# Performance work log

Hardware: AMD Instinct MI355X
Metric: run time of the kernel (lower is better)

## Reference

```python
import jax, jax.numpy as jnp
import numpy as np
import math

N_HEADS = 32
N_KV_HEADS = 8
MAX_SEQ_LEN = 2048


def _rope_cos_sin(seq_len, head_dim, dtype):
    # precompute_freqs_cis: theta=10000, positions 0..seq_len-1 (note: NOT offset by start_pos, faithful to source)
    inv_freq = 1.0 / (10000.0 ** (jnp.arange(0, head_dim, 2, dtype=jnp.float32) / head_dim))
    t = jnp.arange(seq_len, dtype=jnp.float32)
    angles = jnp.outer(t, inv_freq)  # [S, hd/2]
    return jnp.cos(angles).astype(dtype), jnp.sin(angles).astype(dtype)


def _apply_rope(x, cos, sin):
    # x: [B, S, H, hd]; rotate consecutive pairs (llama complex convention)
    B, S, H, hd = x.shape
    xr = x.reshape(B, S, H, hd // 2, 2)
    x1, x2 = xr[..., 0], xr[..., 1]
    c = cos[None, :, None, :]
    s = sin[None, :, None, :]
    o1 = x1 * c - x2 * s
    o2 = x1 * s + x2 * c
    return jnp.stack([o1, o2], axis=-1).reshape(B, S, H, hd)


def setup_inputs() -> dict:
    key = jax.random.key(0)
    ks = jax.random.split(key, 5)
    dim = 4096
    B, S = 1, 2048
    sd = 1.0 / math.sqrt(dim)
    return {
        "x": jax.random.normal(ks[0], (B, S, dim), dtype=jnp.float32),
        "wq": jax.random.normal(ks[1], (4096, 4096), dtype=jnp.float32) * sd,
        "wk": jax.random.normal(ks[2], (1024, 4096), dtype=jnp.float32) * sd,
        "wv": jax.random.normal(ks[3], (1024, 4096), dtype=jnp.float32) * sd,
        "wo": jax.random.normal(ks[4], (4096, 4096), dtype=jnp.float32) * sd,
        "start_pos": 0,
    }


def reference(x, wq, wk, wv, wo, start_pos):
    B, S, D = x.shape
    Hq, Hkv = N_HEADS, N_KV_HEADS
    hd = D // Hq
    n_rep = Hq // Hkv

    xq = (x @ wq.T).reshape(B, S, Hq, hd)
    xk = (x @ wk.T).reshape(B, S, Hkv, hd)
    xv = (x @ wv.T).reshape(B, S, Hkv, hd)

    cos, sin = _rope_cos_sin(S, hd, x.dtype)
    xq = _apply_rope(xq, cos, sin)
    xk = _apply_rope(xk, cos, sin)

    # KV cache append + read back [:, :start_pos+S] (start_pos is a static Python int)
    cache_k = jnp.zeros((B, MAX_SEQ_LEN, Hkv, hd), dtype=x.dtype)
    cache_v = jnp.zeros((B, MAX_SEQ_LEN, Hkv, hd), dtype=x.dtype)
    cache_k = jax.lax.dynamic_update_slice(cache_k, xk, (0, start_pos, 0, 0))
    cache_v = jax.lax.dynamic_update_slice(cache_v, xv, (0, start_pos, 0, 0))
    kv_len = start_pos + S
    keys = cache_k[:, :kv_len]    # [B, K, Hkv, hd]
    values = cache_v[:, :kv_len]

    # GQA repeat_kv: [B, K, Hkv, hd] -> [B, K, Hq, hd]
    keys = jnp.broadcast_to(keys[:, :, :, None, :], (B, kv_len, Hkv, n_rep, hd)).reshape(B, kv_len, Hq, hd)
    values = jnp.broadcast_to(values[:, :, :, None, :], (B, kv_len, Hkv, n_rep, hd)).reshape(B, kv_len, Hq, hd)

    scale = 1.0 / math.sqrt(hd)
    scores = jnp.einsum('bqhd,bkhd->bhqk', xq, keys) * scale  # [B, Hq, S, K]
    # NOTE: source applies NO causal mask — faithful reproduction
    attn = jax.nn.softmax(scores, axis=-1)
    out = jnp.einsum('bhqk,bkhd->bqhd', attn, values).reshape(B, S, Hq * hd)
    return out @ wo.T
```

## Files before the change

### kernel.cpp

```cpp
#include <hip/hip_runtime.h>
#include <hip/hip_bf16.h>

typedef _Float16 f16_t;
typedef unsigned int uint;
typedef __attribute__((ext_vector_type(8))) _Float16 f16x8;
typedef __attribute__((ext_vector_type(4))) _Float16 f16x4;
typedef __attribute__((ext_vector_type(4))) float f32x4;
typedef __attribute__((ext_vector_type(16))) float f32x16;

#define ROPE_C (13.287712379549449f / 64.0f)

__global__ __launch_bounds__(256) void repack_x16(const float* __restrict__ src,
                                                  uint16_t* __restrict__ dh)
{
    const int p  = blockIdx.y;
    const int kb = blockIdx.x;
    const int tid = threadIdx.x;
    const int rr = tid >> 3;
    const int k4 = tid & 7;
    const int slot = k4 >> 1;
    const int so   = (k4 & 1) * 4;
    uint16_t* bh = dh + ((size_t)p * 128 + kb) * 4096;
    #pragma unroll
    for (int it = 0; it < 4; ++it) {
        const int r = it * 32 + rr;
        const float4 v = *reinterpret_cast<const float4*>(
            &src[((size_t)p * 128 + r) * 4096 + kb * 32 + k4 * 4]);
        float f[4] = {v.x, v.y, v.z, v.w};
        f16x4 h;
        #pragma unroll
        for (int e = 0; e < 4; ++e) h[e] = (f16_t)f[e];
        const int pos = r * 32 + ((slot ^ ((r >> 1) & 3)) << 3) + so;
        *reinterpret_cast<f16x4*>(&bh[pos]) = h;
    }
}

__global__ __launch_bounds__(256) void repack_w96_16(const float* __restrict__ wq,
                                                     const float* __restrict__ wk,
                                                     const float* __restrict__ wv,
                                                     uint16_t* __restrict__ dst)
{
    const int kb  = blockIdx.x;
    const int pan = blockIdx.y;
    const int tid = threadIdx.x;
    const int k4 = tid & 7;
    const int slot = k4 >> 1;
    const int so   = (k4 & 1) * 4;
    uint16_t* bh = dst + ((size_t)pan * 128 + kb) * 3072;
    #pragma unroll
    for (int it = 0; it < 3; ++it) {
        const int r = it * 32 + (tid >> 3);
        const int n = pan * 96 + r;
        const float* srow = (n < 4096) ? (wq + (size_t)n * 4096)
                          : (n < 5120) ? (wk + (size_t)(n - 4096) * 4096)
                                       : (wv + (size_t)(n - 5120) * 4096);
        const float4 v = *reinterpret_cast<const float4*>(srow + kb * 32 + k4 * 4);
        float f[4] = {v.x, v.y, v.z, v.w};
        f16x4 h;
        #pragma unroll
        for (int e = 0; e < 4; ++e) h[e] = (f16_t)f[e];
        const int pos = r * 32 + ((slot ^ ((r >> 1) & 3)) << 3) + so;
        *reinterpret_cast<f16x4*>(&bh[pos]) = h;
    }
}

__global__ __launch_bounds__(256) void repack_h16(const float* __restrict__ src,
                                                  uint16_t* __restrict__ dh)
{
    const int p  = blockIdx.y;
    const int kb = blockIdx.x;
    const int tid = threadIdx.x;
    const int rr = tid >> 3;
    const int k4 = tid & 7;
    const int slot = k4 >> 1;
    const int so   = (k4 & 1) * 4;
    uint16_t* bh = dh + ((size_t)p * 128 + kb) * 4096;
    #pragma unroll
    for (int it = 0; it < 4; ++it) {
        const int r = it * 32 + rr;
        const float4 v = *reinterpret_cast<const float4*>(
            &src[((size_t)p * 128 + r) * 4096 + kb * 32 + k4 * 4]);
        float f[4] = {v.x, v.y, v.z, v.w};
        f16x4 h;
        #pragma unroll
        for (int e = 0; e < 4; ++e) h[e] = (f16_t)f[e];
        const int pos = r * 32 + ((slot ^ ((r >> 1) & 3)) << 3) + so;
        *reinterpret_cast<f16x4*>(&bh[pos]) = h;
    }
}

__global__ __launch_bounds__(512) void gemm_qkv9(const uint16_t* __restrict__ xh,
                                                 const uint16_t* __restrict__ wqkv,
                                                 uint16_t* __restrict__ xq16,
                                                 uint16_t* __restrict__ xk16,
                                                 uint16_t* __restrict__ xv16)
{
    __shared__ char lds[2][40960];

    const int bid = blockIdx.x;
    const int swz = (bid & 7) * 64 + (bid >> 3);
    const int by = swz >> 5;
    const int bx = swz & 31;
    const int tid = threadIdx.x;
    const int w = tid >> 6, lane = tid & 63;
    const int wm = w >> 2, wn = w & 3;
    const int fr = lane & 15, s4 = lane >> 4;

    const uint16_t* sp[5];
    int dof[5];
    int stridec[5];
    #pragma unroll
    for (int i = 0; i < 5; ++i) {
        const int c = w + 8 * i;
        if (c < 16) {
            const int kk = c >> 3, inner = c & 7;
            sp[i] = xh + (size_t)by * 524288 + kk * 4096 + inner * 512 + lane * 8;
            dof[i] = c * 1024;
            stridec[i] = 8192;
        } else {
            const int cb = c - 16;
            const int pan = cb / 12, rem = cb % 12;
            const int kk = rem / 6, inner = rem % 6;
            sp[i] = wqkv + (size_t)(bx * 2 + pan) * 393216 + kk * 3072 + inner * 512 + lane * 8;
            dof[i] = 16384 + cb * 1024;
            stridec[i] = 6144;
        }
    }

    f32x4 acc[4][3] = {};

    #pragma unroll
    for (int i = 0; i < 5; ++i)
        __builtin_amdgcn_global_load_lds(
            (const __attribute__((address_space(1))) void*)(sp[i]),
            (__attribute__((address_space(3))) void*)(&lds[0][0] + dof[i]), 16, 0, 0);
    asm volatile("s_waitcnt vmcnt(0)" ::: "memory");
    __builtin_amdgcn_s_barrier();
    __builtin_amdgcn_sched_barrier(0);

    for (int t = 0; t < 64; ++t) {
        const char* b = &lds[t & 1][0];
        if (t + 1 < 64) {
            char* nb = &lds[(t + 1) & 1][0];
            #pragma unroll
            for (int i = 0; i < 5; ++i)
                __builtin_amdgcn_global_load_lds(
                    (const __attribute__((address_space(1))) void*)(sp[i] + (size_t)(t + 1) * stridec[i]),
                    (__attribute__((address_space(3))) void*)(nb + dof[i]), 16, 0, 0);
        }
        #pragma unroll
        for (int kk = 0; kk < 2; ++kk) {
            f16x8 fb[3];
            #pragma unroll
            for (int j = 0; j < 3; ++j) {
                const int cbp = wn * 48 + j * 16 + fr;
                const int pan = (cbp >= 96) ? 1 : 0;
                const int rb = cbp - pan * 96;
                fb[j] = *reinterpret_cast<const f16x8*>(
                    b + 16384 + pan * 12288 + kk * 6144 + rb * 64 + ((s4 ^ ((rb >> 1) & 3)) << 4));
            }
            #pragma unroll
            for (int ri = 0; ri < 4; ++ri) {
                const int rloc = wm * 64 + ri * 16 + fr;
                f16x8 fh = *reinterpret_cast<const f16x8*>(
                    b + kk * 8192 + rloc * 64 + ((s4 ^ ((rloc >> 1) & 3)) << 4));
                __builtin_amdgcn_s_setprio(1);
                #pragma unroll
                for (int j = 0; j < 3; ++j)
                    acc[ri][j] = __builtin_amdgcn_mfma_f32_16x16x32_f16(fh, fb[j], acc[ri][j], 0, 0, 0);
                __builtin_amdgcn_s_setprio(0);
            }
        }
        asm volatile("s_waitcnt vmcnt(0)" ::: "memory");
        __builtin_amdgcn_s_barrier();
        __builtin_amdgcn_sched_barrier(0);
    }

    const int r0 = by * 128 + wm * 64 + s4 * 4;
    const int c0 = bx * 192 + wn * 48 + fr;
    #pragma unroll
    for (int ri = 0; ri < 4; ++ri)
        #pragma unroll
        for (int j = 0; j < 3; ++j) {
            const int col = c0 + j * 16;
            #pragma unroll
            for (int rr = 0; rr < 4; ++rr) {
                const int row = r0 + ri * 16 + rr;
                const f16_t v = (f16_t)acc[ri][j][rr];
                uint16_t bits;
                __builtin_memcpy(&bits, &v, 2);
                if (col < 4096)      xq16[(size_t)row * 4096 + col] = bits;
                else if (col < 5120) xk16[(size_t)row * 1024 + (col - 4096)] = bits;
                else                 xv16[(size_t)row * 1024 + (col - 5120)] = bits;
            }
        }
}

__global__ __launch_bounds__(512) void gemm_out8(const uint16_t* __restrict__ aoh,
                                                 const uint16_t* __restrict__ woh,
                                                 float* __restrict__ out)
{
    __shared__ char lds[2][49152];

    const int bid = blockIdx.x;
    const int swz = (bid & 7) * 32 + (bid >> 3);
    const int by = swz >> 5;
    const int bx = swz & 31;
    const int tid = threadIdx.x;
    const int w = tid >> 6, lane = tid & 63;
    const int wm = w >> 2, wn = w & 3;
    const int fr = lane & 15, s4 = lane >> 4;

    const uint16_t* sp[6];
    int dof[6];
    #pragma unroll
    for (int i = 0; i < 6; ++i) {
        const int c = w + 8 * i;
        if (c < 32) {
            const int pan = c >> 4, sub = c & 15;
            sp[i] = aoh + (size_t)(2 * by + pan) * 524288 + sub * 512 + lane * 8;
            dof[i] = c * 1024;
        } else {
            sp[i] = woh + (size_t)bx * 524288 + (c - 32) * 512 + lane * 8;
            dof[i] = 32768 + (c - 32) * 1024;
        }
    }

    f32x4 acc[8][2] = {};

    #pragma unroll
    for (int i = 0; i < 6; ++i)
        __builtin_amdgcn_global_load_lds(
            (const __attribute__((address_space(1))) void*)(sp[i]),
            (__attribute__((address_space(3))) void*)(&lds[0][0] + dof[i]), 16, 0, 0);
    asm volatile("s_waitcnt vmcnt(0)" ::: "memory");
    __builtin_amdgcn_s_barrier();
    __builtin_amdgcn_sched_barrier(0);

    for (int t = 0; t < 64; ++t) {
        const char* b = &lds[t & 1][0];
        if (t + 1 < 64) {
            char* nb = &lds[(t + 1) & 1][0];
            #pragma unroll
            for (int i = 0; i < 6; ++i)
                __builtin_amdgcn_global_load_lds(
                    (const __attribute__((address_space(1))) void*)(sp[i] + (size_t)(t + 1) * 8192),
                    (__attribute__((address_space(3))) void*)(nb + dof[i]), 16, 0, 0);
        }
        #pragma unroll
        for (int kk = 0; kk < 2; ++kk) {
            f16x8 fb[2];
            #pragma unroll
            for (int j = 0; j < 2; ++j) {
                const int cbp = wn * 32 + j * 16 + fr;
                fb[j] = *reinterpret_cast<const f16x8*>(
                    b + 32768 + kk * 8192 + cbp * 64 + ((s4 ^ ((cbp >> 1) & 3)) << 4));
            }
            #pragma unroll
            for (int p = 0; p < 4; ++p) {
                f16x8 fh[2];
                #pragma unroll
                for (int f = 0; f < 2; ++f) {
                    const int rloc = p * 32 + f * 16 + fr;
                    fh[f] = *reinterpret_cast<const f16x8*>(
                        b + wm * 16384 + kk * 8192 + rloc * 64 + ((s4 ^ ((rloc >> 1) & 3)) << 4));
                }
                __builtin_amdgcn_s_setprio(1);
                #pragma unroll
                for (int f = 0; f < 2; ++f)
                    #pragma unroll
                    for (int j = 0; j < 2; ++j)
                        acc[p * 2 + f][j] = __builtin_amdgcn_mfma_f32_16x16x32_f16(fh[f], fb[j], acc[p * 2 + f][j], 0, 0, 0);
                __builtin_amdgcn_s_setprio(0);
            }
        }
        asm volatile("s_waitcnt vmcnt(0)" ::: "memory");
        __builtin_amdgcn_s_barrier();
        __builtin_amdgcn_sched_barrier(0);
    }

    const int r0 = by * 256 + wm * 128 + s4 * 4;
    const int c0 = bx * 128 + wn * 32 + fr;
    #pragma unroll
    for (int ri = 0; ri < 8; ++ri)
        #pragma unroll
        for (int j = 0; j < 2; ++j)
            #pragma unroll
            for (int rr = 0; rr < 4; ++rr)
                out[(size_t)(r0 + ri * 16 + rr) * 4096 + c0 + j * 16] = acc[ri][j][rr];
}

__global__ __launch_bounds__(256) void conv_kv(const uint16_t* __restrict__ xk16,
                                               const uint16_t* __restrict__ xv16,
                                               uint16_t* __restrict__ kvg)
{
    __shared__ float V[32][129];
    const int t = blockIdx.x;
    const int h = blockIdx.y;
    const int tid = threadIdx.x;
    uint16_t* tile = kvg + ((size_t)(h * 64 + t)) * 8192;

    #pragma unroll
    for (int i = 0; i < 4; ++i) {
        const int v = i * 256 + tid;
        const int row = v >> 5, c4 = (v & 31) * 4;
        f16x4 hv = *reinterpret_cast<const f16x4*>(&xv16[(size_t)(t * 32 + row) * 1024 + h * 128 + c4]);
        #pragma unroll
        for (int e = 0; e < 4; ++e) V[row][c4 + e] = (float)hv[e];
    }

    {
        const int r = tid >> 3;
        const int d0 = (tid & 7) * 16;
        const int pos_ = t * 32 + r;
        float f[16];
        const uint16_t* kr = &xk16[(size_t)pos_ * 1024 + h * 128 + d0];
        f16x8 k0 = *reinterpret_cast<const f16x8*>(kr);
        f16x8 k1 = *reinterpret_cast<const f16x8*>(kr + 8);
        #pragma unroll
        for (int e = 0; e < 8; ++e) { f[e] = (float)k0[e]; f[8 + e] = (float)k1[e]; }
        #pragma unroll
        for (int i = 0; i < 8; ++i) {
            const int j = (d0 >> 1) + i;
            const float invf = exp2f(-(float)j * ROPE_C);
            const float ang = (float)pos_ * invf;
            float sn, cs;
            __sincosf(ang, &sn, &cs);
            const float x1 = f[2 * i], x2 = f[2 * i + 1];
            f[2 * i]     = x1 * cs - x2 * sn;
            f[2 * i + 1] = x1 * sn + x2 * cs;
        }
        #pragma unroll
        for (int cc = 0; cc < 2; ++cc) {
            f16x8 hv;
            #pragma unroll
            for (int e = 0; e < 8; ++e) hv[e] = (f16_t)f[cc * 8 + e];
            const int c = (d0 >> 3) + cc;
            const int pos = r * 128 + ((c ^ (r & 15)) << 3);
            *reinterpret_cast<f16x8*>(&tile[pos]) = hv;
        }
    }
    __syncthreads();
    {
        const int d = tid >> 1;
        const int k0 = (tid & 1) * 16;
        float g[16];
        #pragma unroll
        for (int j = 0; j < 16; ++j) g[j] = V[k0 + j][d];
        #pragma unroll
        for (int cc = 0; cc < 2; ++cc) {
            f16x8 hv;
            #pragma unroll
            for (int e = 0; e < 8; ++e) hv[e] = (f16_t)g[cc * 8 + e];
            const int c = (k0 >> 3) + cc;
            const int pos = 4096 + d * 32 + ((c ^ (d & 3)) << 3);
            *reinterpret_cast<f16x8*>(&tile[pos]) = hv;
        }
    }
}

__device__ __forceinline__ uint cvtpkh(float lo, float hi) {
    uint r;
    asm("v_cvt_pkrtz_f16_f32 %0, %1, %2" : "=v"(r) : "v"(lo), "v"(hi));
    return r;
}
__device__ __forceinline__ void permswap(uint& a, uint& b) {
    asm("v_permlane32_swap_b32 %0, %1" : "+v"(a), "+v"(b));
}
__device__ __forceinline__ f16x8 pack4h(uint w0, uint w1, uint w2, uint w3) {
    union { uint u[4]; f16x8 v; } t;
    t.u[0] = w0; t.u[1] = w1; t.u[2] = w2; t.u[3] = w3;
    return t.v;
}

__global__ __launch_bounds__(512, 2) void attn_mfma(const uint16_t* __restrict__ xq16,
                                                    const uint16_t* __restrict__ kvg,
                                                    uint16_t* __restrict__ aoh)
{
    __shared__ char lds[2][16384];

    const int b = blockIdx.x;
    const int kvh = b & 7;
    const int r = b >> 3;
    const int h = kvh * 4 + (r & 3);
    const int q0 = (r >> 2) * 256;
    const int tid = threadIdx.x;
    const int w = tid >> 6;
    const int lane = tid & 63;
    const int ln31 = lane & 31;
    const int hi = lane >> 5;

    const int q = q0 + w * 32 + ln31;
    const uint16_t* qrow = xq16 + (size_t)q * 4096 + h * 128;
    f16x8 Qh[8];
    #pragma unroll
    for (int ks = 0; ks < 8; ++ks) {
        const int dbase = ks * 16 + hi * 8;
        f16x8 raw = *reinterpret_cast<const f16x8*>(qrow + dbase);
        float f[8];
        #pragma unroll
        for (int e = 0; e < 8; ++e) f[e] = (float)raw[e];
        #pragma unroll
        for (int i = 0; i < 4; ++i) {
            const int j = (dbase >> 1) + i;
            const float invf = exp2f(-(float)j * ROPE_C);
            const float ang = (float)q * invf;
            float sn, cs;
            __sincosf(ang, &sn, &cs);
            const float x1 = f[2 * i], x2 = f[2 * i + 1];
            f[2 * i]     = (x1 * cs - x2 * sn) * 0.08838834764831845f;
            f[2 * i + 1] = (x1 * sn + x2 * cs) * 0.08838834764831845f;
        }
        #pragma unroll
        for (int e = 0; e < 8; ++e) Qh[ks][e] = (f16_t)f[e];
    }

    const char* gkv = (const char*)kvg + (size_t)kvh * 64 * 16384;

    f32x16 oacc[4] = {{}, {}, {}, {}};
    float m = -3.0e38f, l = 0.f;

    {
        #pragma unroll
        for (int i = 0; i < 2; ++i) {
            const int chunk = i * 8 + w;
            __builtin_amdgcn_global_load_lds(
                (const __attribute__((address_space(1))) void*)(gkv + chunk * 1024 + lane * 16),
                (__attribute__((address_space(3))) void*)(&lds[0][chunk * 1024]),
                16, 0, 0);
        }
    }

    for (int t = 0; t < 64; ++t) {
        __syncthreads();
        if (t + 1 < 64) {
            const char* g = gkv + (size_t)(t + 1) * 16384;
            const int buf = (t + 1) & 1;
            #pragma unroll
            for (int i = 0; i < 2; ++i) {
                const int chunk = i * 8 + w;
                __builtin_amdgcn_global_load_lds(
                    (const __attribute__((address_space(1))) void*)(g + chunk * 1024 + lane * 16),
                    (__attribute__((address_space(3))) void*)(&lds[buf][chunk * 1024]),
                    16, 0, 0);
            }
        }
        const int cur = t & 1;
        const char* Kf = lds[cur];
        const char* Vf = lds[cur] + 8192;

        f32x16 s0 = {}, s1 = {};
        __builtin_amdgcn_s_setprio(1);
        #pragma unroll
        for (int ks = 0; ks < 8; ++ks) {
            const int byt = ln31 * 256 + ((ks * 32 + hi * 16) ^ ((ln31 & 15) << 4));
            f16x8 a = *reinterpret_cast<const f16x8*>(Kf + byt);
            if (ks & 1) s1 = __builtin_amdgcn_mfma_f32_32x32x16_f16(a, Qh[ks], s1, 0, 0, 0);
            else        s0 = __builtin_amdgcn_mfma_f32_32x32x16_f16(a, Qh[ks], s0, 0, 0, 0);
        }
        __builtin_amdgcn_s_setprio(0);
        f32x16 s = s0 + s1;

        float pmax = s[0];
        #pragma unroll
        for (int jj = 1; jj < 16; ++jj) pmax = fmaxf(pmax, s[jj]);
        pmax = fmaxf(pmax, __shfl_xor(pmax, 32));
        if (!__all(pmax - m <= 8.0f)) {
            const float mnew = fmaxf(m, pmax);
            const float corr = __expf(m - mnew);
            l *= corr;
            #pragma unroll
            for (int dt = 0; dt < 4; ++dt) oacc[dt] *= corr;
            m = mnew;
        }
        float psum = 0.f;
        #pragma unroll
        for (int jj = 0; jj < 16; ++jj) {
            float pv = __expf(s[jj] - m);
            s[jj] = pv;
            psum += pv;
        }
        psum += __shfl_xor(psum, 32);
        l += psum;

        #pragma unroll
        for (int ks = 0; ks < 2; ++ks) {
            const int b0 = ks * 8;
            uint wa = cvtpkh(s[b0 + 0], s[b0 + 1]);
            uint wb = cvtpkh(s[b0 + 2], s[b0 + 3]);
            uint wc = cvtpkh(s[b0 + 4], s[b0 + 5]);
            uint wd = cvtpkh(s[b0 + 6], s[b0 + 7]);
            permswap(wa, wc); permswap(wb, wd);
            f16x8 Pf = pack4h(wa, wb, wc, wd);
            __builtin_amdgcn_s_setprio(1);
            #pragma unroll
            for (int dt = 0; dt < 4; ++dt) {
                const int row = dt * 32 + ln31;
                const int byt = row * 64 + ((ks * 32 + hi * 16) ^ ((row & 3) << 4));
                f16x8 vh = *reinterpret_cast<const f16x8*>(Vf + byt);
                oacc[dt] = __builtin_amdgcn_mfma_f32_32x32x16_f16(vh, Pf, oacc[dt], 0, 0, 0);
            }
            __builtin_amdgcn_s_setprio(0);
        }
    }

    const float invl = 1.0f / l;
    const int p   = q >> 7;
    const int rr_ = q & 127;
    const int rsw = (rr_ >> 1) & 3;
    #pragma unroll
    for (int dt = 0; dt < 4; ++dt) {
        const int kb = h * 4 + dt;
        uint16_t* bh = aoh + ((size_t)p * 128 + kb) * 4096;
        #pragma unroll
        for (int g4 = 0; g4 < 4; ++g4) {
            f16x4 hv;
            #pragma unroll
            for (int e = 0; e < 4; ++e)
                hv[e] = (f16_t)(oacc[dt][g4 * 4 + e] * invl);
            const int pos = rr_ * 32 + ((g4 ^ rsw) << 3) + 4 * hi;
            *reinterpret_cast<f16x4*>(&bh[pos]) = hv;
        }
    }
}

extern "C" void kernel_launch(void* const* d_in, const int* in_sizes, int n_in,
                              void* d_out, int out_size, void* d_ws, size_t ws_size,
                              hipStream_t stream)
{
    const float* x  = (const float*)d_in[0];
    const float* wq = (const float*)d_in[1];
    const float* wk = (const float*)d_in[2];
    const float* wv = (const float*)d_in[3];
    const float* wo = (const float*)d_in[4];
    float* out = (float*)d_out;

    float* ws = (float*)d_ws;
    uint16_t* xq16 = (uint16_t*)ws;
    uint16_t* kvg  = (uint16_t*)(ws + 8388608);
    uint16_t* xk16 = (uint16_t*)(ws + 12582912);
    uint16_t* xv16 = (uint16_t*)(ws + 14680064);
    uint16_t* aoh  = (uint16_t*)(ws + 12582912);
    uint16_t* xh   = (uint16_t*)(ws + 20971520);
    uint16_t* wqkv = (uint16_t*)(ws + 29360128);
    uint16_t* woh  = (uint16_t*)(ws + 41943040);

    dim3 blk(256);
    repack_x16   <<<dim3(128, 16), blk, 0, stream>>>(x, xh);
    repack_w96_16<<<dim3(128, 64), blk, 0, stream>>>(wq, wk, wv, wqkv);
    gemm_qkv9    <<<dim3(512), dim3(512), 0, stream>>>(xh, wqkv, xq16, xk16, xv16);
    repack_h16   <<<dim3(128, 32), blk, 0, stream>>>(wo, woh);
    conv_kv      <<<dim3(64, 8), blk, 0, stream>>>(xk16, xv16, kvg);
    attn_mfma    <<<dim3(256), dim3(512), 0, stream>>>(xq16, kvg, aoh);
    gemm_out8    <<<dim3(256), dim3(512), 0, stream>>>(aoh, woh, out);
}
```

Baseline: 366.3 us.

## Fold wo repack into attention launch and remap GEMM tiles per XCD

The separate wo-to-fp16 repack kernel is removed. Its work now runs in 4096 extra blocks appended to the attention launch, so the bandwidth-bound conversion can fill CUs left idle by the 256 attention blocks and one launch is saved. Both GEMMs also get a new block-index mapping that gives each XCD a contiguous 2D tile patch, aiming for better L2 reuse of A and B panels. The risk is that the repack blocks compete with attention blocks for CUs and memory bandwidth, and the new mapping may change cache behaviour unpredictably.

New measurement: 350.7 us. -4.2%, faster.

```diff
diff --git a/kernel.cpp b/kernel.cpp
--- a/kernel.cpp
+++ b/kernel.cpp
@@ -64,31 +64,6 @@
     }
 }
 
-__global__ __launch_bounds__(256) void repack_h16(const float* __restrict__ src,
-                                                  uint16_t* __restrict__ dh)
-{
-    const int p  = blockIdx.y;
-    const int kb = blockIdx.x;
-    const int tid = threadIdx.x;
-    const int rr = tid >> 3;
-    const int k4 = tid & 7;
-    const int slot = k4 >> 1;
-    const int so   = (k4 & 1) * 4;
-    uint16_t* bh = dh + ((size_t)p * 128 + kb) * 4096;
-    #pragma unroll
-    for (int it = 0; it < 4; ++it) {
-        const int r = it * 32 + rr;
-        const float4 v = *reinterpret_cast<const float4*>(
-            &src[((size_t)p * 128 + r) * 4096 + kb * 32 + k4 * 4]);
-        float f[4] = {v.x, v.y, v.z, v.w};
-        f16x4 h;
-        #pragma unroll
-        for (int e = 0; e < 4; ++e) h[e] = (f16_t)f[e];
-        const int pos = r * 32 + ((slot ^ ((r >> 1) & 3)) << 3) + so;
-        *reinterpret_cast<f16x4*>(&bh[pos]) = h;
-    }
-}
-
 __global__ __launch_bounds__(512) void gemm_qkv9(const uint16_t* __restrict__ xh,
                                                  const uint16_t* __restrict__ wqkv,
                                                  uint16_t* __restrict__ xq16,
@@ -98,9 +73,10 @@
     __shared__ char lds[2][40960];
 
     const int bid = blockIdx.x;
-    const int swz = (bid & 7) * 64 + (bid >> 3);
-    const int by = swz >> 5;
-    const int bx = swz & 31;
+    const int xcd = bid & 7;
+    const int i_  = bid >> 3;
+    const int by = (xcd & 1) * 8 + (i_ & 7);
+    const int bx = (xcd >> 1) * 8 + (i_ >> 3);
     const int tid = threadIdx.x;
     const int w = tid >> 6, lane = tid & 63;
     const int wm = w >> 2, wn = w & 3;
@@ -203,9 +179,10 @@
     __shared__ char lds[2][49152];
 
     const int bid = blockIdx.x;
-    const int swz = (bid & 7) * 32 + (bid >> 3);
-    const int by = swz >> 5;
-    const int bx = swz & 31;
+    const int xcd = bid & 7;
+    const int i_  = bid >> 3;
+    const int by = (xcd & 1) * 4 + (i_ & 3);
+    const int bx = (xcd >> 1) * 8 + (i_ >> 2);
     const int tid = threadIdx.x;
     const int w = tid >> 6, lane = tid & 63;
     const int wm = w >> 2, wn = w & 3;
@@ -375,9 +352,38 @@
 
 __global__ __launch_bounds__(512, 2) void attn_mfma(const uint16_t* __restrict__ xq16,
                                                     const uint16_t* __restrict__ kvg,
-                                                    uint16_t* __restrict__ aoh)
+                                                    uint16_t* __restrict__ aoh,
+                                                    const float* __restrict__ wo,
+                                                    uint16_t* __restrict__ woh)
 {
     __shared__ char lds[2][16384];
+
+    if (blockIdx.x >= 256) {
+        const int rid = blockIdx.x - 256;
+        const int p  = rid >> 7;
+        const int kb = rid & 127;
+        const int tid = threadIdx.x;
+        const int t2 = tid & 255;
+        const int half = tid >> 8;
+        const int rr = t2 >> 3;
+        const int k4 = t2 & 7;
+        const int slot = k4 >> 1;
+        const int so   = (k4 & 1) * 4;
+        uint16_t* bh = woh + ((size_t)p * 128 + kb) * 4096;
+        #pragma unroll
+        for (int it = 0; it < 2; ++it) {
+            const int r = (half * 2 + it) * 32 + rr;
+            const float4 v = *reinterpret_cast<const float4*>(
+                &wo[((size_t)p * 128 + r) * 4096 + kb * 32 + k4 * 4]);
+            float f[4] = {v.x, v.y, v.z, v.w};
+            f16x4 h;
+            #pragma unroll
+            for (int e = 0; e < 4; ++e) h[e] = (f16_t)f[e];
+            const int pos = r * 32 + ((slot ^ ((r >> 1) & 3)) << 3) + so;
+            *reinterpret_cast<f16x4*>(&bh[pos]) = h;
+        }
+        return;
+    }
 
     const int b = blockIdx.x;
     const int kvh = b & 7;
@@ -549,8 +555,7 @@
     repack_x16   <<<dim3(128, 16), blk, 0, stream>>>(x, xh);
     repack_w96_16<<<dim3(128, 64), blk, 0, stream>>>(wq, wk, wv, wqkv);
     gemm_qkv9    <<<dim3(512), dim3(512), 0, stream>>>(xh, wqkv, xq16, xk16, xv16);
-    repack_h16   <<<dim3(128, 32), blk, 0, stream>>>(wo, woh);
     conv_kv      <<<dim3(64, 8), blk, 0, stream>>>(xk16, xv16, kvg);
-    attn_mfma    <<<dim3(256), dim3(512), 0, stream>>>(xq16, kvg, aoh);
+    attn_mfma    <<<dim3(4352), dim3(512), 0, stream>>>(xq16, kvg, aoh, wo, woh);
     gemm_out8    <<<dim3(256), dim3(512), 0, stream>>>(aoh, woh, out);
 }
```
